# Kernel optimization log

Hardware: AMD Instinct MI355X
Metric: run time of the kernel (lower is better)

## Reference

```python
import jax, jax.numpy as jnp
import numpy as np

N = 50000       # nodes
E = 800000      # directed edges (before self-loops)
D_IN = 128
H = 32          # hidden width, heads=1 (PyG SuperGATConv defaults)
D_OUT = 16
L = 15          # stacked SuperGATConv layers
NEG_SLOPE = 0.2


def setup_inputs() -> dict:
    key = jax.random.key(0)
    ks = jax.random.split(key, 8)
    s_in = 1.0 / np.sqrt(D_IN)
    s_h = 1.0 / np.sqrt(H)
    return dict(
        x=jax.random.normal(ks[0], (N, D_IN), jnp.float32),
        edge_index=jax.random.randint(ks[1], (2, E), 0, N, jnp.int32),
        W0=jax.random.normal(ks[2], (D_IN, H), jnp.float32) * s_in,
        b0=jnp.zeros((H,), jnp.float32),
        Ws=jax.random.normal(ks[3], (L, H, H), jnp.float32) * s_h,
        att_l=jax.random.normal(ks[4], (L, H), jnp.float32) * s_h,
        att_r=jax.random.normal(ks[5], (L, H), jnp.float32) * s_h,
        bs=jnp.zeros((L, H), jnp.float32),
        W16=jax.random.normal(ks[6], (H, D_OUT), jnp.float32) * s_h,
        b16=jnp.zeros((D_OUT,), jnp.float32),
    )


def _supergat(h, src, dst, W, al, ar, b):
    # One SuperGATConv (attention_type='MX', heads=1, concat) forward.
    hp = h @ W                          # [N, H] transformed features
    hj = hp[src]                        # [E', H] source (message) features
    hi = hp[dst]                        # [E', H] destination features
    logits = jnp.sum(hi * hj, axis=-1)  # MX dot-product logits
    alpha = hj @ al + hi @ ar           # GAT-style additive scores
    alpha = alpha * jax.nn.sigmoid(logits)
    alpha = jnp.where(alpha >= 0, alpha, NEG_SLOPE * alpha)  # leaky_relu
    # segment softmax over destination nodes
    amax = jax.ops.segment_max(alpha, dst, num_segments=N)
    ex = jnp.exp(alpha - amax[dst])
    den = jax.ops.segment_sum(ex, dst, num_segments=N)
    coef = ex / den[dst]
    out = jax.ops.segment_sum(hj * coef[:, None], dst, num_segments=N)
    return out + b


def reference(x, edge_index, W0, b0, Ws, att_l, att_r, bs, W16, b16):
    # PyG SuperGATConv adds self-loops by default
    loops = jnp.arange(N, dtype=edge_index.dtype)
    src = jnp.concatenate([edge_index[0], loops])
    dst = jnp.concatenate([edge_index[1], loops])
    h = x @ W0 + b0                     # conv0: Linear(in, 32)

    def step(h, p):
        W, al, ar, b = p
        return jax.nn.relu(_supergat(h, src, dst, W, al, ar, b)), None

    h, _ = jax.lax.scan(step, h, (Ws, att_l, att_r, bs))
    return h @ W16 + b16                # conv16: Linear(32, out)
```

## Files before the change

### kernel.cpp

```cpp
#include <hip/hip_runtime.h>
#include <hip/hip_fp16.h>
#include <cmath>
#include <cstring>

#define NN 50000
#define EE 800000
#define ET 850000
#define PADCAP 1004544
#define NBK 831
#define EBINS 196
#define DB 512
#define NB 50

__global__ void k_fill(int* __restrict__ p){
  int i = blockIdx.x*256 + threadIdx.x;
  p[i] = NN;
}

__global__ void k_permfill(int* __restrict__ perm){
  int i = blockIdx.x*256 + threadIdx.x;
  perm[i] = NN;
}

__global__ __launch_bounds__(1024) void k_ebhist(const int* __restrict__ ei,
                                                 int* __restrict__ ebh){
  __shared__ int hist[EBINS];
  int t = threadIdx.x, b = blockIdx.x;
  if (t < EBINS) hist[t] = 0;
  __syncthreads();
  int e = b*1024 + t;
  if (e < ET){
    int d = (e < EE) ? ei[EE + e] : (e - EE);
    atomicAdd(&hist[d >> 8], 1);
  }
  __syncthreads();
  if (t < EBINS) ebh[t*NBK + b] = hist[t];
}

__global__ __launch_bounds__(1024) void k_escan1(const int* __restrict__ ebh,
                                                 int* __restrict__ ebhoff,
                                                 int* __restrict__ btot){
  __shared__ int tmp[1024];
  int bin = blockIdx.x, t = threadIdx.x;
  int v = (t < NBK) ? ebh[bin*NBK + t] : 0;
  int inc = v;
  for (int off = 1; off < 1024; off <<= 1){
    tmp[t] = inc; __syncthreads();
    int add = (t >= off) ? tmp[t - off] : 0;
    __syncthreads();
    inc += add;
  }
  if (t < NBK) ebhoff[bin*NBK + t] = inc - v;
  if (t == 1023) btot[bin] = inc;
}

__global__ __launch_bounds__(256) void k_escan2(const int* __restrict__ btot,
                                                int* __restrict__ bbase){
  __shared__ int tmp[256];
  int t = threadIdx.x;
  int v = (t < EBINS) ? btot[t] : 0;
  int inc = v;
  for (int off = 1; off < 256; off <<= 1){
    tmp[t] = inc; __syncthreads();
    int add = (t >= off) ? tmp[t - off] : 0;
    __syncthreads();
    inc += add;
  }
  if (t < EBINS) bbase[t] = inc - v;
  if (t == 255) bbase[EBINS] = inc;
}

__global__ __launch_bounds__(1024) void k_ebin(const int* __restrict__ ei,
                                               const int* __restrict__ ebhoff,
                                               const int* __restrict__ bbase,
                                               int2* __restrict__ ebuf){
  __shared__ int hist[EBINS];
  int t = threadIdx.x, b = blockIdx.x;
  if (t < EBINS) hist[t] = 0;
  __syncthreads();
  int e = b*1024 + t;
  if (e < ET){
    int s, d;
    if (e < EE){ s = ei[e]; d = ei[EE + e]; } else { s = d = e - EE; }
    int bin = d >> 8;
    int rank = atomicAdd(&hist[bin], 1);
    int pos = bbase[bin] + ebhoff[bin*NBK + b] + rank;
    ebuf[pos] = make_int2(s, d);
  }
}

__global__ __launch_bounds__(1024) void k_ecnt(const int2* __restrict__ ebuf,
                                               const int* __restrict__ bbase,
                                               int* __restrict__ count){
  __shared__ int cnt[256];
  int t = threadIdx.x, bin = blockIdx.x;
  if (t < 256) cnt[t] = 0;
  __syncthreads();
  int rb = bbase[bin], re = bbase[bin+1];
  for (int i = rb + t; i < re; i += 1024) atomicAdd(&cnt[ebuf[i].y - (bin << 8)], 1);
  __syncthreads();
  int idx = (bin << 8) + t;
  if (t < 256 && idx < NN) count[idx] = cnt[t];
}

__global__ void k_bsum(const int* __restrict__ count, int* __restrict__ bsums){
  int i = blockIdx.x*256 + threadIdx.x;
  int v = (i < NN) ? ((count[i] + 3) & ~3) : 0;
  #pragma unroll
  for (int m = 1; m < 64; m <<= 1) v += __shfl_xor(v, m);
  __shared__ int ws[4];
  if ((threadIdx.x & 63) == 0) ws[threadIdx.x >> 6] = v;
  __syncthreads();
  if (threadIdx.x == 0) bsums[blockIdx.x] = ws[0] + ws[1] + ws[2] + ws[3];
}

__global__ void k_bscan(const int* __restrict__ bsums, int* __restrict__ boffs, int nb){
  __shared__ int tmp[256];
  int t = threadIdx.x;
  int self = (t < nb) ? bsums[t] : 0;
  int v = self;
  for (int off = 1; off < 256; off <<= 1){
    tmp[t] = v; __syncthreads();
    int add = (t >= off) ? tmp[t - off] : 0;
    __syncthreads();
    v += add;
  }
  if (t < nb) boffs[t] = v - self;
}

__global__ void k_scan(const int* __restrict__ count, const int* __restrict__ boffs,
                       int* __restrict__ offs){
  __shared__ int tmp[256];
  int t = threadIdx.x;
  int gid = blockIdx.x*256 + t;
  int self = (gid < NN) ? ((count[gid] + 3) & ~3) : 0;
  int v = self;
  for (int off = 1; off < 256; off <<= 1){
    tmp[t] = v; __syncthreads();
    int add = (t >= off) ? tmp[t - off] : 0;
    __syncthreads();
    v += add;
  }
  int excl = v - self + boffs[blockIdx.x];
  if (gid < NN) offs[gid] = excl;
  if (gid == NN-1) offs[NN] = excl + self;
}

__global__ __launch_bounds__(1024) void k_escatter(const int2* __restrict__ ebuf,
                                                   const int* __restrict__ bbase,
                                                   const int* __restrict__ offs,
                                                   int* __restrict__ srcCSR){
  __shared__ int cur[256];
  int t = threadIdx.x, bin = blockIdx.x;
  if (t < 256){ int idx = (bin << 8) + t; cur[t] = (idx < NN) ? offs[idx] : 0; }
  __syncthreads();
  int rb = bbase[bin], re = bbase[bin+1];
  for (int i = rb + t; i < re; i += 1024){
    int2 e = ebuf[i];
    int p = atomicAdd(&cur[e.y - (bin << 8)], 1);
    srcCSR[p] = e.x;
  }
}

__global__ __launch_bounds__(1024) void k_dhist_blk(const int* __restrict__ count,
                                                    int* __restrict__ blockhist){
  __shared__ int hist[DB];
  int t = threadIdx.x, b = blockIdx.x;
  if (t < DB) hist[t] = 0;
  __syncthreads();
  int i = b*1024 + t;
  if (i < NN){
    int deg = count[i]; if (deg > DB-1) deg = DB-1;
    atomicAdd(&hist[DB-1-deg], 1);
  }
  __syncthreads();
  if (t < DB) blockhist[t*NB + b] = hist[t];
}

__global__ __launch_bounds__(DB) void k_dcol(const int* __restrict__ blockhist,
                                             int* __restrict__ blockoffs,
                                             int* __restrict__ dbase){
  int k = threadIdx.x;
  int run = 0;
  #pragma unroll 5
  for (int b = 0; b < NB; ++b){
    int v = blockhist[k*NB + b];
    blockoffs[k*NB + b] = run;
    run += v;
  }
  __shared__ int tmp[DB];
  int v = run;
  for (int off = 1; off < DB; off <<= 1){
    tmp[k] = v; __syncthreads();
    int add = (k >= off) ? tmp[k - off] : 0;
    __syncthreads();
    v += add;
  }
  dbase[k] = v - run;
}

__global__ __launch_bounds__(1024) void k_dscatter_blk(const int* __restrict__ count,
                                                       const int* __restrict__ blockoffs,
                                                       const int* __restrict__ dbase,
                                                       int* __restrict__ perm){
  __shared__ int hist[DB];
  int t = threadIdx.x, b = blockIdx.x;
  if (t < DB) hist[t] = 0;
  __syncthreads();
  int i = b*1024 + t;
  if (i < NN){
    int deg = count[i]; if (deg > DB-1) deg = DB-1;
    int bin = DB-1-deg;
    int rank = atomicAdd(&hist[bin], 1);
    int pos = dbase[bin] + blockoffs[bin*NB + b] + rank;
    perm[pos] = i;
  }
}

__device__ __forceinline__ void cvt8(uint4 r, float* v){
  __half2 h;
  memcpy(&h, &r.x, 4); float2 f = __half22float2(h); v[0]=f.x; v[1]=f.y;
  memcpy(&h, &r.y, 4); f = __half22float2(h); v[2]=f.x; v[3]=f.y;
  memcpy(&h, &r.z, 4); f = __half22float2(h); v[4]=f.x; v[5]=f.y;
  memcpy(&h, &r.w, 4); f = __half22float2(h); v[6]=f.x; v[7]=f.y;
}
__device__ __forceinline__ unsigned pack_h2(float x, float y){
  __half2 h = __floats2half2_rn(x, y);
  unsigned u; memcpy(&u, &h, 4); return u;
}

__global__ __launch_bounds__(256) void k_prologue(
    const float* __restrict__ x, const float* __restrict__ W0, const float* __restrict__ b0,
    const float* __restrict__ Ws0, __half* __restrict__ hp_out){
  __shared__ __align__(16) float xs[128*33];
  __shared__ __align__(16) float w0s[128*32];
  __shared__ __align__(16) float w1s[32*32];
  int t = threadIdx.x, b = blockIdx.x;
  #pragma unroll
  for (int k = 0; k < 4; ++k){
    int i = t + k*256;
    int n = i >> 5, j4 = (i & 31) << 2;
    int r = b*32 + n;
    const float4* src = (const float4*)(x + (size_t)((r < NN) ? r : 0)*128);
    float4 v = src[i & 31];
    xs[(j4+0)*33 + n] = v.x;
    xs[(j4+1)*33 + n] = v.y;
    xs[(j4+2)*33 + n] = v.z;
    xs[(j4+3)*33 + n] = v.w;
  }
  {
    const float4* w04 = (const float4*)W0;
    float4* dst = (float4*)w0s;
    #pragma unroll
    for (int k = 0; k < 4; ++k) dst[t + k*256] = w04[t + k*256];
    ((float4*)w1s)[t] = ((const float4*)Ws0)[t];
  }
  __syncthreads();
  int nloc = t >> 3, c8 = t & 7;
  float4 acc = ((const float4*)b0)[c8];
  const float* xcol = xs + nloc;
  const float4* w0r = (const float4*)w0s + c8;
  #pragma unroll 8
  for (int j = 0; j < 128; ++j){
    float xv = xcol[j*33];
    float4 wv = w0r[j*8];
    acc.x += xv*wv.x; acc.y += xv*wv.y; acc.z += xv*wv.z; acc.w += xv*wv.w;
  }
  __syncthreads();
  float* hs = w0s;
  ((float4*)(hs + nloc*36))[c8] = acc;
  float4 o = {0.f,0.f,0.f,0.f};
  const float* hrow = hs + nloc*36;
  const float4* w1r = (const float4*)w1s + c8;
  #pragma unroll 8
  for (int j = 0; j < 32; ++j){
    float hv = hrow[j];
    float4 wv = w1r[j*8];
    o.x += hv*wv.x; o.y += hv*wv.y; o.z += hv*wv.z; o.w += hv*wv.w;
  }
  int n = b*32 + nloc;
  if (n < NN){
    uint2 st; st.x = pack_h2(o.x, o.y); st.y = pack_h2(o.z, o.w);
    *(uint2*)(hp_out + (size_t)n*32 + (c8 << 2)) = st;
  }
  if (b == 0 && t < 32) hp_out[(size_t)NN*32 + t] = __float2half(0.f);
}

__global__ __launch_bounds__(256) void k_layer(
    const __half* __restrict__ hp,
    const int* __restrict__ offs, const int* __restrict__ srcCSR, const int* __restrict__ perm,
    const float* __restrict__ bcur, const float* __restrict__ alc, const float* __restrict__ arc,
    const float* __restrict__ Wn, const float* __restrict__ b16,
    __half* __restrict__ hp_out, float* __restrict__ final_out, int last){
  __shared__ __align__(16) float wl[1024];
  __shared__ __align__(16) float xb[64*36];
  int t = threadIdx.x;
  int nW = last ? 512 : 1024;
  for (int i = t; i < nW; i += 256) wl[i] = Wn[i];
  int lane = t & 63;
  int li = lane & 3;
  int slot = t >> 2;
  int d = perm[blockIdx.x*64 + slot];
  int beg = offs[d];
  int lenP = offs[d+1] - beg;
  int ng = (d < NN) ? (lenP >> 2) : 0;
  float hpd[8];
  cvt8(*(const uint4*)(hp + ((size_t)d << 5) + (li << 3)), hpd);
  float4 ala = ((const float4*)alc)[2*li], alb = ((const float4*)alc)[2*li+1];
  float4 ara = ((const float4*)arc)[2*li], arb = ((const float4*)arc)[2*li+1];
  float hrd = hpd[0]*ara.x + hpd[1]*ara.y + hpd[2]*ara.z + hpd[3]*ara.w
            + hpd[4]*arb.x + hpd[5]*arb.y + hpd[6]*arb.z + hpd[7]*arb.w;
  hrd += __shfl_xor(hrd, 1); hrd += __shfl_xor(hrd, 2);

  int maxg = ng;
  #pragma unroll
  for (int m = 1; m < 64; m <<= 1) maxg = max(maxg, __shfl_xor(maxg, m));

  auto LD4 = [&](int g)->int4{
    int4 q = *(const int4*)(srcCSR + beg + (g << 2));
    if (g >= ng){ q.x = NN; q.y = NN; q.z = NN; q.w = NN; }
    return q;
  };
  auto ROW = [&](int s)->uint4{
    return *(const uint4*)(hp + ((size_t)s << 5) + (li << 3));
  };
  float acc[8] = {0.f,0.f,0.f,0.f,0.f,0.f,0.f,0.f};
  float den = 0.f;
  auto EDGE = [&](uint4 r, int s){
    float v[8];
    cvt8(r, v);
    float p = v[0]*hpd[0] + v[1]*hpd[1] + v[2]*hpd[2] + v[3]*hpd[3]
            + v[4]*hpd[4] + v[5]*hpd[5] + v[6]*hpd[6] + v[7]*hpd[7];
    float q = v[0]*ala.x + v[1]*ala.y + v[2]*ala.z + v[3]*ala.w
            + v[4]*alb.x + v[5]*alb.y + v[6]*alb.z + v[7]*alb.w;
    p += __shfl_xor(p, 1); p += __shfl_xor(p, 2);
    q += __shfl_xor(q, 1); q += __shfl_xor(q, 2);
    float a = (q + hrd) * (1.f/(1.f + __expf(-p)));
    a = fmaxf(a, 0.2f*a);
    float e = __expf(a);
    e = (s < NN) ? e : 0.f;
    den += e;
    #pragma unroll
    for (int k = 0; k < 8; ++k) acc[k] += v[k]*e;
  };

  int4 qA = LD4(0);
  uint4 rA0=ROW(qA.x), rA1=ROW(qA.y), rA2=ROW(qA.z), rA3=ROW(qA.w);
  int4 qB = LD4(1);

  for (int g = 0; g < maxg; g += 2){
    uint4 rB0=ROW(qB.x), rB1=ROW(qB.y), rB2=ROW(qB.z), rB3=ROW(qB.w);
    int4 qN = LD4(g + 2);
    EDGE(rA0,qA.x); EDGE(rA1,qA.y); EDGE(rA2,qA.z); EDGE(rA3,qA.w);
    rA0=ROW(qN.x); rA1=ROW(qN.y); rA2=ROW(qN.z); rA3=ROW(qN.w);
    qA = qN;
    int4 qB2 = LD4(g + 3);
    EDGE(rB0,qB.x); EDGE(rB1,qB.y); EDGE(rB2,qB.z); EDGE(rB3,qB.w);
    qB = qB2;
  }

  float rden = 1.f/den;
  const float4* bc4 = (const float4*)bcur;
  float4 ba = bc4[2*li], bb = bc4[2*li+1];
  float* hrow = xb + slot*36;
  {
    float4 h0, h1;
    h0.x = fmaxf(acc[0]*rden + ba.x, 0.f);
    h0.y = fmaxf(acc[1]*rden + ba.y, 0.f);
    h0.z = fmaxf(acc[2]*rden + ba.z, 0.f);
    h0.w = fmaxf(acc[3]*rden + ba.w, 0.f);
    h1.x = fmaxf(acc[4]*rden + bb.x, 0.f);
    h1.y = fmaxf(acc[5]*rden + bb.y, 0.f);
    h1.z = fmaxf(acc[6]*rden + bb.z, 0.f);
    h1.w = fmaxf(acc[7]*rden + bb.w, 0.f);
    *((float4*)hrow + 2*li) = h0;
    *((float4*)hrow + 2*li + 1) = h1;
  }
  __syncthreads();

  const float4* wl4 = (const float4*)wl;
  if (!last){
    float o[8] = {0.f,0.f,0.f,0.f,0.f,0.f,0.f,0.f};
    #pragma unroll
    for (int k = 0; k < 32; ++k){
      float hk = hrow[k];
      float4 wa = wl4[k*8 + 2*li];
      float4 wb = wl4[k*8 + 2*li + 1];
      o[0]+=hk*wa.x; o[1]+=hk*wa.y; o[2]+=hk*wa.z; o[3]+=hk*wa.w;
      o[4]+=hk*wb.x; o[5]+=hk*wb.y; o[6]+=hk*wb.z; o[7]+=hk*wb.w;
    }
    if (d < NN){
      uint4 st;
      st.x = pack_h2(o[0], o[1]); st.y = pack_h2(o[2], o[3]);
      st.z = pack_h2(o[4], o[5]); st.w = pack_h2(o[6], o[7]);
      *(uint4*)(hp_out + ((size_t)d << 5) + (li << 3)) = st;
    }
    if (blockIdx.x == 0){
      if (t < 32) hp_out[(size_t)NN*32 + t] = __float2half(0.f);
    }
  } else {
    float4 o = ((const float4*)b16)[li];
    #pragma unroll
    for (int k = 0; k < 32; ++k){
      float hk = hrow[k];
      float4 wv = wl4[k*4 + li];
      o.x += hk*wv.x; o.y += hk*wv.y; o.z += hk*wv.z; o.w += hk*wv.w;
    }
    if (d < NN) *((float4*)(final_out + (size_t)d*16) + li) = o;
  }
}

extern "C" void kernel_launch(void* const* d_in, const int* in_sizes, int n_in,
                              void* d_out, int out_size, void* d_ws, size_t ws_size,
                              hipStream_t stream){
  const float* x   = (const float*)d_in[0];
  const int*   ei  = (const int*)  d_in[1];
  const float* W0  = (const float*)d_in[2];
  const float* b0  = (const float*)d_in[3];
  const float* Ws  = (const float*)d_in[4];
  const float* al  = (const float*)d_in[5];
  const float* ar  = (const float*)d_in[6];
  const float* bs  = (const float*)d_in[7];
  const float* W16 = (const float*)d_in[8];
  const float* b16 = (const float*)d_in[9];
  float* out = (float*)d_out;

  char* w = (char*)d_ws;
  int* count     = (int*)w;   w += 50176*sizeof(int);
  int* offs      = (int*)w;   w += 50432*sizeof(int);
  int* srcCSR    = (int*)w;   w += (size_t)PADCAP*sizeof(int);
  int* bsums     = (int*)w;   w += 256*sizeof(int);
  int* boffs     = (int*)w;   w += 256*sizeof(int);
  int* perm      = (int*)w;   w += 50176*sizeof(int);
  int* blockhist = (int*)w;   w += DB*NB*sizeof(int);
  int* blockoffs = (int*)w;   w += DB*NB*sizeof(int);
  int* dbase     = (int*)w;   w += DB*sizeof(int);
  int* ebh       = (int*)w;   w += (size_t)EBINS*NBK*sizeof(int) + 16;
  int* ebhoff    = (int*)w;   w += (size_t)EBINS*NBK*sizeof(int) + 16;
  int* btot      = (int*)w;   w += 256*sizeof(int);
  int* bbase     = (int*)w;   w += 256*sizeof(int);
  int2* ebuf     = (int2*)w;  w += (size_t)(NBK*1024)*sizeof(int2);
  __half* hpA  = (__half*)w; w += (size_t)(NN+16)*32*sizeof(__half);
  __half* hpB  = (__half*)w; w += (size_t)(NN+16)*32*sizeof(__half);

  k_fill    <<<PADCAP/256, 256, 0, stream>>>(srcCSR);
  k_permfill<<<196, 256, 0, stream>>>(perm);
  k_ebhist  <<<NBK, 1024, 0, stream>>>(ei, ebh);
  k_escan1  <<<EBINS, 1024, 0, stream>>>(ebh, ebhoff, btot);
  k_escan2  <<<1, 256, 0, stream>>>(btot, bbase);
  k_ebin    <<<NBK, 1024, 0, stream>>>(ei, ebhoff, bbase, ebuf);
  k_ecnt    <<<EBINS, 1024, 0, stream>>>(ebuf, bbase, count);
  k_bsum    <<<196, 256, 0, stream>>>(count, bsums);
  k_bscan   <<<1, 256, 0, stream>>>(bsums, boffs, 196);
  k_scan    <<<196, 256, 0, stream>>>(count, boffs, offs);
  k_escatter<<<EBINS, 1024, 0, stream>>>(ebuf, bbase, offs, srcCSR);
  k_dhist_blk   <<<NB, 1024, 0, stream>>>(count, blockhist);
  k_dcol        <<<1,  DB,   0, stream>>>(blockhist, blockoffs, dbase);
  k_dscatter_blk<<<NB, 1024, 0, stream>>>(count, blockoffs, dbase, perm);

  k_prologue<<<1563, 256, 0, stream>>>(x, W0, b0, Ws, hpA);

  int nblk = 50048 / 64;
  for (int l = 0; l < 15; ++l){
    const __half* hin = (l & 1) ? hpB : hpA;
    __half* hout = (l & 1) ? hpA : hpB;
    int last = (l == 14);
    const float* Wn  = last ? W16 : (Ws + (size_t)(l+1)*1024);
    k_layer<<<nblk, 256, 0, stream>>>(hin, offs, srcCSR, perm,
                                      bs + (size_t)l*32,
                                      al + (size_t)l*32, ar + (size_t)l*32,
                                      Wn, b16,
                                      hout, out, last);
  }
}
```

Before: 436.3 us.

## Pack edge buffer, drop fill kernels, deepen gather prefetch pipeline in layer kernel

Packs each binned edge into one int (source in the low 16 bits, local destination in the high bits), halving binning-buffer traffic. Removes the srcCSR and perm fill kernels: k_scan writes the padding slots and k_layer guards out-of-range perm reads. The layer kernel's neighbor gather changes from a two-group unrolled loop to a rolling three-stage prefetch that processes one group per iteration. This can hide more gather latency but raises register pressure and adds per-iteration loop overhead.

```diff
diff --git a/kernel.cpp b/kernel.cpp
--- a/kernel.cpp
+++ b/kernel.cpp
@@ -11,16 +11,6 @@
 #define EBINS 196
 #define DB 512
 #define NB 50
-
-__global__ void k_fill(int* __restrict__ p){
-  int i = blockIdx.x*256 + threadIdx.x;
-  p[i] = NN;
-}
-
-__global__ void k_permfill(int* __restrict__ perm){
-  int i = blockIdx.x*256 + threadIdx.x;
-  perm[i] = NN;
-}
 
 __global__ __launch_bounds__(1024) void k_ebhist(const int* __restrict__ ei,
                                                  int* __restrict__ ebh){
@@ -73,7 +63,7 @@
 __global__ __launch_bounds__(1024) void k_ebin(const int* __restrict__ ei,
                                                const int* __restrict__ ebhoff,
                                                const int* __restrict__ bbase,
-                                               int2* __restrict__ ebuf){
+                                               int* __restrict__ ebuf){
   __shared__ int hist[EBINS];
   int t = threadIdx.x, b = blockIdx.x;
   if (t < EBINS) hist[t] = 0;
@@ -85,11 +75,11 @@
     int bin = d >> 8;
     int rank = atomicAdd(&hist[bin], 1);
     int pos = bbase[bin] + ebhoff[bin*NBK + b] + rank;
-    ebuf[pos] = make_int2(s, d);
-  }
-}
-
-__global__ __launch_bounds__(1024) void k_ecnt(const int2* __restrict__ ebuf,
+    ebuf[pos] = s | ((d & 255) << 16);
+  }
+}
+
+__global__ __launch_bounds__(1024) void k_ecnt(const int* __restrict__ ebuf,
                                                const int* __restrict__ bbase,
                                                int* __restrict__ count){
   __shared__ int cnt[256];
@@ -97,7 +87,7 @@
   if (t < 256) cnt[t] = 0;
   __syncthreads();
   int rb = bbase[bin], re = bbase[bin+1];
-  for (int i = rb + t; i < re; i += 1024) atomicAdd(&cnt[ebuf[i].y - (bin << 8)], 1);
+  for (int i = rb + t; i < re; i += 1024) atomicAdd(&cnt[(ebuf[i] >> 16) & 255], 1);
   __syncthreads();
   int idx = (bin << 8) + t;
   if (t < 256 && idx < NN) count[idx] = cnt[t];
@@ -129,11 +119,12 @@
 }
 
 __global__ void k_scan(const int* __restrict__ count, const int* __restrict__ boffs,
-                       int* __restrict__ offs){
+                       int* __restrict__ offs, int* __restrict__ srcCSR){
   __shared__ int tmp[256];
   int t = threadIdx.x;
   int gid = blockIdx.x*256 + t;
-  int self = (gid < NN) ? ((count[gid] + 3) & ~3) : 0;
+  int cnt = (gid < NN) ? count[gid] : 0;
+  int self = (cnt + 3) & ~3;
   int v = self;
   for (int off = 1; off < 256; off <<= 1){
     tmp[t] = v; __syncthreads();
@@ -142,11 +133,14 @@
     v += add;
   }
   int excl = v - self + boffs[blockIdx.x];
-  if (gid < NN) offs[gid] = excl;
+  if (gid < NN){
+    offs[gid] = excl;
+    for (int k = cnt; k < self; ++k) srcCSR[excl + k] = NN;
+  }
   if (gid == NN-1) offs[NN] = excl + self;
 }
 
-__global__ __launch_bounds__(1024) void k_escatter(const int2* __restrict__ ebuf,
+__global__ __launch_bounds__(1024) void k_escatter(const int* __restrict__ ebuf,
                                                    const int* __restrict__ bbase,
                                                    const int* __restrict__ offs,
                                                    int* __restrict__ srcCSR){
@@ -156,9 +150,9 @@
   __syncthreads();
   int rb = bbase[bin], re = bbase[bin+1];
   for (int i = rb + t; i < re; i += 1024){
-    int2 e = ebuf[i];
-    int p = atomicAdd(&cur[e.y - (bin << 8)], 1);
-    srcCSR[p] = e.x;
+    int v = ebuf[i];
+    int p = atomicAdd(&cur[(v >> 16) & 255], 1);
+    srcCSR[p] = v & 0xFFFF;
   }
 }
 
@@ -300,10 +294,10 @@
   int lane = t & 63;
   int li = lane & 3;
   int slot = t >> 2;
-  int d = perm[blockIdx.x*64 + slot];
-  int beg = offs[d];
-  int lenP = offs[d+1] - beg;
-  int ng = (d < NN) ? (lenP >> 2) : 0;
+  int gs = blockIdx.x*64 + slot;
+  int d = (gs < NN) ? perm[gs] : NN;
+  int beg = (d < NN) ? offs[d] : 0;
+  int ng  = (d < NN) ? ((offs[d+1] - beg) >> 2) : 0;
   float hpd[8];
   cvt8(*(const uint4*)(hp + ((size_t)d << 5) + (li << 3)), hpd);
   float4 ala = ((const float4*)alc)[2*li], alb = ((const float4*)alc)[2*li+1];
@@ -344,19 +338,19 @@
     for (int k = 0; k < 8; ++k) acc[k] += v[k]*e;
   };
 
-  int4 qA = LD4(0);
-  uint4 rA0=ROW(qA.x), rA1=ROW(qA.y), rA2=ROW(qA.z), rA3=ROW(qA.w);
-  int4 qB = LD4(1);
-
-  for (int g = 0; g < maxg; g += 2){
-    uint4 rB0=ROW(qB.x), rB1=ROW(qB.y), rB2=ROW(qB.z), rB3=ROW(qB.w);
-    int4 qN = LD4(g + 2);
-    EDGE(rA0,qA.x); EDGE(rA1,qA.y); EDGE(rA2,qA.z); EDGE(rA3,qA.w);
-    rA0=ROW(qN.x); rA1=ROW(qN.y); rA2=ROW(qN.z); rA3=ROW(qN.w);
-    qA = qN;
-    int4 qB2 = LD4(g + 3);
-    EDGE(rB0,qB.x); EDGE(rB1,qB.y); EDGE(rB2,qB.z); EDGE(rB3,qB.w);
-    qB = qB2;
+  int4 q0 = LD4(0);
+  uint4 r00=ROW(q0.x), r01=ROW(q0.y), r02=ROW(q0.z), r03=ROW(q0.w);
+  int4 q1 = LD4(1);
+  uint4 r10=ROW(q1.x), r11=ROW(q1.y), r12=ROW(q1.z), r13=ROW(q1.w);
+  int4 q2 = LD4(2);
+
+  for (int g = 0; g < maxg; ++g){
+    uint4 r20=ROW(q2.x), r21=ROW(q2.y), r22=ROW(q2.z), r23=ROW(q2.w);
+    int4 q3 = LD4(g + 3);
+    EDGE(r00,q0.x); EDGE(r01,q0.y); EDGE(r02,q0.z); EDGE(r03,q0.w);
+    r00=r10; r01=r11; r02=r12; r03=r13;
+    r10=r20; r11=r21; r12=r22; r13=r23;
+    q0=q1; q1=q2; q2=q3;
   }
 
   float rden = 1.f/den;
@@ -439,12 +433,10 @@
   int* ebhoff    = (int*)w;   w += (size_t)EBINS*NBK*sizeof(int) + 16;
   int* btot      = (int*)w;   w += 256*sizeof(int);
   int* bbase     = (int*)w;   w += 256*sizeof(int);
-  int2* ebuf     = (int2*)w;  w += (size_t)(NBK*1024)*sizeof(int2);
+  int* ebuf      = (int*)w;   w += (size_t)(NBK*1024)*sizeof(int);
   __half* hpA  = (__half*)w; w += (size_t)(NN+16)*32*sizeof(__half);
   __half* hpB  = (__half*)w; w += (size_t)(NN+16)*32*sizeof(__half);
 
-  k_fill    <<<PADCAP/256, 256, 0, stream>>>(srcCSR);
-  k_permfill<<<196, 256, 0, stream>>>(perm);
   k_ebhist  <<<NBK, 1024, 0, stream>>>(ei, ebh);
   k_escan1  <<<EBINS, 1024, 0, stream>>>(ebh, ebhoff, btot);
   k_escan2  <<<1, 256, 0, stream>>>(btot, bbase);
@@ -452,7 +444,7 @@
   k_ecnt    <<<EBINS, 1024, 0, stream>>>(ebuf, bbase, count);
   k_bsum    <<<196, 256, 0, stream>>>(count, bsums);
   k_bscan   <<<1, 256, 0, stream>>>(bsums, boffs, 196);
-  k_scan    <<<196, 256, 0, stream>>>(count, boffs, offs);
+  k_scan    <<<196, 256, 0, stream>>>(count, boffs, offs, srcCSR);
   k_escatter<<<EBINS, 1024, 0, stream>>>(ebuf, bbase, offs, srcCSR);
   k_dhist_blk   <<<NB, 1024, 0, stream>>>(count, blockhist);
   k_dcol        <<<1,  DB,   0, stream>>>(blockhist, blockoffs, dbase);
```

Result: slower. 480.0 us (+10.0%).
